# Kernel optimization log

Hardware: AMD Instinct MI355X
Metric: run time of the kernel (lower is better)

Reference implementation:

```python
import jax, jax.numpy as jnp
import numpy as np

D = 2048
N_EXPERTS = 64
K = 2


def setup_inputs() -> dict:
    key = jax.random.key(0)
    kx, kw = jax.random.split(key)
    x = jax.random.normal(kx, (4, 4096, D), dtype=jnp.float32)
    # xavier_uniform for Linear(d, n_experts): bound = sqrt(6/(fan_in+fan_out))
    bound = float(np.sqrt(6.0 / (D + N_EXPERTS)))
    W = jax.random.uniform(kw, (N_EXPERTS, D), dtype=jnp.float32, minval=-bound, maxval=bound)
    b = jnp.zeros((N_EXPERTS,), dtype=jnp.float32)
    return {"x": x, "W": W, "b": b}


def reference(x, W, b):
    # logits: [B, S, E]  (eval mode: no noise)
    logits = jnp.einsum("bsd,ed->bse", x, W) + b
    topk_vals, topk_idx = jax.lax.top_k(logits, K)  # [B, S, K]
    gates = jax.nn.softmax(topk_vals, axis=-1)
    return gates, topk_idx
```

## Files before the change

kernel.cpp:

```cpp
#include <hip/hip_runtime.h>
#include <math.h>

#define DD 2048
#define EE 64
#define TM 32
#define BK 64
#define NCHUNK (DD / BK)
#define THREADS 256
#define LDSX 34
#define LDSW 68

__global__ __launch_bounds__(THREADS) void router_kernel(
    const float* __restrict__ x, const float* __restrict__ W,
    const float* __restrict__ bias_g, float* __restrict__ out, int n_tokens)
{
    __shared__ __attribute__((aligned(16))) float xs[BK * LDSX];
    __shared__ __attribute__((aligned(16))) float ws[BK * LDSW];
    __shared__ __attribute__((aligned(16))) float logits[TM * (EE + 1)];

    const int tid = threadIdx.x;
    const int tx  = tid & 15;
    const int ty  = tid >> 4;
    const int tBase = blockIdx.x * TM;

    const int xt = tid >> 3;
    const int xc = tid & 7;
    const int we = tid >> 2;
    const int wc = tid & 3;

    const float* xrow = x + (size_t)(tBase + xt) * DD;
    const float* wrow = W + (size_t)we * DD;

    float acc[2][4];
#pragma unroll
    for (int t = 0; t < 2; ++t)
#pragma unroll
        for (int j = 0; j < 4; ++j) acc[t][j] = 0.f;

    const float4 bv4 = *(const float4*)&bias_g[tx * 4];

    float4 rx[2], rw[4];

#define LOAD_TILES(k0)                                                       \
    {                                                                        \
        _Pragma("unroll")                                                    \
        for (int p = 0; p < 2; ++p)                                          \
            rx[p] = *(const float4*)&xrow[(k0) + 4 * (xc + 8 * p)];          \
        _Pragma("unroll")                                                    \
        for (int p = 0; p < 4; ++p)                                          \
            rw[p] = *(const float4*)&wrow[(k0) + 4 * (wc + 4 * p)];          \
    }

    LOAD_TILES(0);

    for (int c = 0; c < NCHUNK; ++c) {
        __syncthreads();

#pragma unroll
        for (int p = 0; p < 2; ++p) {
            const int k = 4 * (xc + 8 * p);
            xs[(k + 0) * LDSX + xt] = rx[p].x;
            xs[(k + 1) * LDSX + xt] = rx[p].y;
            xs[(k + 2) * LDSX + xt] = rx[p].z;
            xs[(k + 3) * LDSX + xt] = rx[p].w;
        }
#pragma unroll
        for (int p = 0; p < 4; ++p) {
            const int k = 4 * (wc + 4 * p);
            ws[(k + 0) * LDSW + we] = rw[p].x;
            ws[(k + 1) * LDSW + we] = rw[p].y;
            ws[(k + 2) * LDSW + we] = rw[p].z;
            ws[(k + 3) * LDSW + we] = rw[p].w;
        }
        __syncthreads();

        if (c + 1 < NCHUNK) {
            const int k0n = (c + 1) * BK;
            LOAD_TILES(k0n);
        }

#pragma unroll
        for (int k = 0; k < BK; ++k) {
            const float2 xv = *(const float2*)&xs[k * LDSX + ty * 2];
            const float4 wv = *(const float4*)&ws[k * LDSW + tx * 4];
            acc[0][0] += xv.x * wv.x; acc[0][1] += xv.x * wv.y;
            acc[0][2] += xv.x * wv.z; acc[0][3] += xv.x * wv.w;
            acc[1][0] += xv.y * wv.x; acc[1][1] += xv.y * wv.y;
            acc[1][2] += xv.y * wv.z; acc[1][3] += xv.y * wv.w;
        }
    }

    __syncthreads();
#pragma unroll
    for (int t = 0; t < 2; ++t) {
        const int row = (ty * 2 + t) * (EE + 1);
        logits[row + tx * 4 + 0] = acc[t][0] + bv4.x;
        logits[row + tx * 4 + 1] = acc[t][1] + bv4.y;
        logits[row + tx * 4 + 2] = acc[t][2] + bv4.z;
        logits[row + tx * 4 + 3] = acc[t][3] + bv4.w;
    }
    __syncthreads();

    if (tid < TM) {
        const float* lrow = &logits[tid * (EE + 1)];
        float v1 = -INFINITY, v2 = -INFINITY;
        int   i1 = 0, i2 = 0;
        for (int e = 0; e < EE; ++e) {
            const float v = lrow[e];
            if (v > v1) { v2 = v1; i2 = i1; v1 = v; i1 = e; }
            else if (v > v2) { v2 = v; i2 = e; }
        }
        const float ed = expf(v2 - v1);
        const float inv = 1.f / (1.f + ed);
        const int tok = tBase + tid;
        out[tok * 2 + 0] = inv;
        out[tok * 2 + 1] = ed * inv;
        float* oidx = out + (size_t)2 * n_tokens;
        oidx[tok * 2 + 0] = (float)i1;
        oidx[tok * 2 + 1] = (float)i2;
    }
}

extern "C" void kernel_launch(void* const* d_in, const int* in_sizes, int n_in,
                              void* d_out, int out_size, void* d_ws, size_t ws_size,
                              hipStream_t stream) {
    const float* x = (const float*)d_in[0];
    const float* W = (const float*)d_in[1];
    const float* b = (const float*)d_in[2];
    float* out = (float*)d_out;

    const int n_tokens = in_sizes[0] / DD;
    const int n_blocks = n_tokens / TM;

    router_kernel<<<n_blocks, THREADS, 0, stream>>>(x, W, b, out, n_tokens);
}
```

Baseline: 235.4 us.

## Use split-fp16 MFMA for router GEMM with double-buffered LDS

Replaces the scalar FP32 FMA inner loop with fp16 MFMA 16x16x32 instructions. Each fp32 operand is scaled and split into hi and lo fp16 parts, and four MFMAs per product pair approximate fp32 accuracy. Staging moves to a two-buffer LDS scheme with one barrier per chunk so global loads and the fp16 split overlap compute. Risks include precision loss from the fp16 split, which could flip top-k ordering on near ties, extra conversion work, and a larger LDS footprint.

Result: faster. 203.2 us (-13.7%).

```diff
diff --git a/kernel.cpp b/kernel.cpp
--- a/kernel.cpp
+++ b/kernel.cpp
@@ -7,20 +7,34 @@
 #define BK 64
 #define NCHUNK (DD / BK)
 #define THREADS 256
-#define LDSX 34
-#define LDSW 68
+
+#define ROWB 144
+#define XPLANE (TM * ROWB)
+#define WPLANE (EE * ROWB)
+#define BUFB   (2 * XPLANE + 2 * WPLANE)
+
+typedef _Float16 f16x8 __attribute__((ext_vector_type(8)));
+typedef _Float16 f16x4 __attribute__((ext_vector_type(4)));
+typedef float    f32x4 __attribute__((ext_vector_type(4)));
+
+__device__ static inline void split_f4(const float4 v, f16x4& hi, f16x4& lo) {
+    const float S = 32.f;
+    const float a0 = v.x * S, a1 = v.y * S, a2 = v.z * S, a3 = v.w * S;
+    const _Float16 h0 = (_Float16)a0, h1 = (_Float16)a1;
+    const _Float16 h2 = (_Float16)a2, h3 = (_Float16)a3;
+    hi = (f16x4){h0, h1, h2, h3};
+    lo = (f16x4){(_Float16)(a0 - (float)h0), (_Float16)(a1 - (float)h1),
+                 (_Float16)(a2 - (float)h2), (_Float16)(a3 - (float)h3)};
+}
 
 __global__ __launch_bounds__(THREADS) void router_kernel(
     const float* __restrict__ x, const float* __restrict__ W,
     const float* __restrict__ bias_g, float* __restrict__ out, int n_tokens)
 {
-    __shared__ __attribute__((aligned(16))) float xs[BK * LDSX];
-    __shared__ __attribute__((aligned(16))) float ws[BK * LDSW];
+    __shared__ __attribute__((aligned(16))) char  lds[2 * BUFB];
     __shared__ __attribute__((aligned(16))) float logits[TM * (EE + 1)];
 
-    const int tid = threadIdx.x;
-    const int tx  = tid & 15;
-    const int ty  = tid >> 4;
+    const int tid   = threadIdx.x;
     const int tBase = blockIdx.x * TM;
 
     const int xt = tid >> 3;
@@ -28,76 +42,92 @@
     const int we = tid >> 2;
     const int wc = tid & 3;
 
-    const float* xrow = x + (size_t)(tBase + xt) * DD;
-    const float* wrow = W + (size_t)we * DD;
-
-    float acc[2][4];
-#pragma unroll
-    for (int t = 0; t < 2; ++t)
-#pragma unroll
-        for (int j = 0; j < 4; ++j) acc[t][j] = 0.f;
-
-    const float4 bv4 = *(const float4*)&bias_g[tx * 4];
+    const float* xrow = x + (size_t)(tBase + xt) * DD + xc * 4;
+    const float* wrow = W + (size_t)we * DD + wc * 4;
 
     float4 rx[2], rw[4];
 
-#define LOAD_TILES(k0)                                                       \
-    {                                                                        \
-        _Pragma("unroll")                                                    \
-        for (int p = 0; p < 2; ++p)                                          \
-            rx[p] = *(const float4*)&xrow[(k0) + 4 * (xc + 8 * p)];          \
-        _Pragma("unroll")                                                    \
-        for (int p = 0; p < 4; ++p)                                          \
-            rw[p] = *(const float4*)&wrow[(k0) + 4 * (wc + 4 * p)];          \
+#define LOADX(c) { _Pragma("unroll") for (int p = 0; p < 2; ++p) \
+        rx[p] = *(const float4*)&xrow[(c) * BK + p * 32]; }
+#define LOADW(c) { _Pragma("unroll") for (int q = 0; q < 4; ++q) \
+        rw[q] = *(const float4*)&wrow[(c) * BK + q * 16]; }
+
+#define WRITE_STAGE(buf) { \
+    char* base = lds + (buf) * BUFB; \
+    char* xh = base; char* xl = base + XPLANE; \
+    char* wh = base + 2 * XPLANE; char* wl = base + 2 * XPLANE + WPLANE; \
+    _Pragma("unroll") for (int p = 0; p < 2; ++p) { \
+        f16x4 hi, lo; split_f4(rx[p], hi, lo); \
+        const int off = xt * ROWB + (xc + 8 * p) * 8; \
+        *(f16x4*)(xh + off) = hi; *(f16x4*)(xl + off) = lo; \
+    } \
+    _Pragma("unroll") for (int q = 0; q < 4; ++q) { \
+        f16x4 hi, lo; split_f4(rw[q], hi, lo); \
+        const int off = we * ROWB + (wc + 4 * q) * 8; \
+        *(f16x4*)(wh + off) = hi; *(f16x4*)(wl + off) = lo; \
+    } }
+
+    const int wv   = tid >> 6;
+    const int lane = tid & 63;
+    const int mtile = wv & 1;
+    const int ngrp  = wv >> 1;
+    const int r16  = lane & 15;
+    const int kg   = lane >> 4;
+
+    const int aoff  = (mtile * 16 + r16) * ROWB + kg * 16;
+    const int boff0 = ((ngrp * 2 + 0) * 16 + r16) * ROWB + kg * 16;
+    const int boff1 = ((ngrp * 2 + 1) * 16 + r16) * ROWB + kg * 16;
+
+    f32x4 acc0 = {0.f, 0.f, 0.f, 0.f};
+    f32x4 acc1 = {0.f, 0.f, 0.f, 0.f};
+
+#define COMPUTE(buf) { \
+    char* base = lds + (buf) * BUFB; \
+    char* xh = base; char* xl = base + XPLANE; \
+    char* wh = base + 2 * XPLANE; char* wl = base + 2 * XPLANE + WPLANE; \
+    _Pragma("unroll") for (int ks = 0; ks < 2; ++ks) { \
+        const int ko = ks * 64; \
+        const f16x8 ah  = *(const f16x8*)(xh + aoff  + ko); \
+        const f16x8 al  = *(const f16x8*)(xl + aoff  + ko); \
+        const f16x8 bh0 = *(const f16x8*)(wh + boff0 + ko); \
+        const f16x8 bl0 = *(const f16x8*)(wl + boff0 + ko); \
+        const f16x8 bh1 = *(const f16x8*)(wh + boff1 + ko); \
+        const f16x8 bl1 = *(const f16x8*)(wl + boff1 + ko); \
+        acc0 = __builtin_amdgcn_mfma_f32_16x16x32_f16(ah, bh0, acc0, 0, 0, 0); \
+        acc0 = __builtin_amdgcn_mfma_f32_16x16x32_f16(al, bh0, acc0, 0, 0, 0); \
+        acc0 = __builtin_amdgcn_mfma_f32_16x16x32_f16(ah, bl0, acc0, 0, 0, 0); \
+        acc0 = __builtin_amdgcn_mfma_f32_16x16x32_f16(al, bl0, acc0, 0, 0, 0); \
+        acc1 = __builtin_amdgcn_mfma_f32_16x16x32_f16(ah, bh1, acc1, 0, 0, 0); \
+        acc1 = __builtin_amdgcn_mfma_f32_16x16x32_f16(al, bh1, acc1, 0, 0, 0); \
+        acc1 = __builtin_amdgcn_mfma_f32_16x16x32_f16(ah, bl1, acc1, 0, 0, 0); \
+        acc1 = __builtin_amdgcn_mfma_f32_16x16x32_f16(al, bl1, acc1, 0, 0, 0); \
+    } }
+
+    LOADX(0); LOADW(0);
+    WRITE_STAGE(0);
+    LOADX(1); LOADW(1);
+
+    int cur = 0;
+    for (int c = 0; c < NCHUNK; ++c) {
+        __syncthreads();
+        COMPUTE(cur);
+        if (c + 1 < NCHUNK) {
+            WRITE_STAGE(cur ^ 1);
+            if (c + 2 < NCHUNK) { LOADX(c + 2); LOADW(c + 2); }
+        }
+        cur ^= 1;
     }
 
-    LOAD_TILES(0);
-
-    for (int c = 0; c < NCHUNK; ++c) {
-        __syncthreads();
-
+    const int col0 = ngrp * 32 + r16;
+    const int col1 = ngrp * 32 + 16 + r16;
+    const float b0 = bias_g[col0];
+    const float b1 = bias_g[col1];
+    const float INV = 1.f / 1024.f;
+    const int rbase = mtile * 16 + kg * 4;
 #pragma unroll
-        for (int p = 0; p < 2; ++p) {
-            const int k = 4 * (xc + 8 * p);
-            xs[(k + 0) * LDSX + xt] = rx[p].x;
-            xs[(k + 1) * LDSX + xt] = rx[p].y;
-            xs[(k + 2) * LDSX + xt] = rx[p].z;
-            xs[(k + 3) * LDSX + xt] = rx[p].w;
-        }
-#pragma unroll
-        for (int p = 0; p < 4; ++p) {
-            const int k = 4 * (wc + 4 * p);
-            ws[(k + 0) * LDSW + we] = rw[p].x;
-            ws[(k + 1) * LDSW + we] = rw[p].y;
-            ws[(k + 2) * LDSW + we] = rw[p].z;
-            ws[(k + 3) * LDSW + we] = rw[p].w;
-        }
-        __syncthreads();
-
-        if (c + 1 < NCHUNK) {
-            const int k0n = (c + 1) * BK;
-            LOAD_TILES(k0n);
-        }
-
-#pragma unroll
-        for (int k = 0; k < BK; ++k) {
-            const float2 xv = *(const float2*)&xs[k * LDSX + ty * 2];
-            const float4 wv = *(const float4*)&ws[k * LDSW + tx * 4];
-            acc[0][0] += xv.x * wv.x; acc[0][1] += xv.x * wv.y;
-            acc[0][2] += xv.x * wv.z; acc[0][3] += xv.x * wv.w;
-            acc[1][0] += xv.y * wv.x; acc[1][1] += xv.y * wv.y;
-            acc[1][2] += xv.y * wv.z; acc[1][3] += xv.y * wv.w;
-        }
-    }
-
-    __syncthreads();
-#pragma unroll
-    for (int t = 0; t < 2; ++t) {
-        const int row = (ty * 2 + t) * (EE + 1);
-        logits[row + tx * 4 + 0] = acc[t][0] + bv4.x;
-        logits[row + tx * 4 + 1] = acc[t][1] + bv4.y;
-        logits[row + tx * 4 + 2] = acc[t][2] + bv4.z;
-        logits[row + tx * 4 + 3] = acc[t][3] + bv4.w;
+    for (int r = 0; r < 4; ++r) {
+        logits[(rbase + r) * (EE + 1) + col0] = acc0[r] * INV + b0;
+        logits[(rbase + r) * (EE + 1) + col1] = acc1[r] * INV + b1;
     }
     __syncthreads();
 
```
